# Kernel optimization log

Hardware: AMD Instinct MI355X
Metric: run time of the kernel (lower is better)

## Reference

```python
import jax, jax.numpy as jnp
import numpy as np

N, H, W, KB, CTRL, MEM, L, NMOD = 256, 14, 14, 512, 512, 512, 8, 9
TEMP = 1.0
EPS = 1e-12


def _l2norm(x):
    # torch F.normalize(p=2, dim=-1, eps=1e-12)
    return x / jnp.maximum(jnp.linalg.norm(x, axis=-1, keepdims=True), EPS)


def _spatial_softmax(att):  # [N,H,W,1]
    n = att.shape[0]
    return jax.nn.softmax(att.reshape(n, -1), axis=1).reshape(att.shape)


def _extract_softmax_avg(kb, att_raw):  # -> [N,KB]
    return (kb * _spatial_softmax(att_raw)).sum((1, 2))


def _move_bw(ptr):
    # conv1d with kernel [0,0,1], pad 1 => shift left (pop); guard keeps mass at slot 0
    new = jnp.pad(ptr[:, 1:], ((0, 0), (0, 1)))
    return new.at[:, 0].add(ptr[:, 0])


def _move_fw(ptr):
    # conv1d with kernel [1,0,0], pad 1 => shift right (push); guard keeps mass at slot L-1
    new = jnp.pad(ptr[:, :-1], ((0, 0), (1, 0)))
    return new.at[:, -1].add(ptr[:, -1])


def _read(stk, ptr):  # [N,H,W,L],[N,L] -> [N,H,W,1]
    return (stk * ptr[:, None, None, :]).sum(-1, keepdims=True)


def _write(stk, ptr, att):
    p = ptr[:, None, None, :]
    return att * p + stk * (1.0 - p)


def _sharpen(ptr):
    return jax.nn.softmax(ptr / TEMP, axis=1)


def setup_inputs() -> dict:
    key = jax.random.key(0)
    ks = jax.random.split(key, 16)

    def lin(k, fan_in, shape):
        return (jax.random.normal(k, shape, jnp.float32) / np.sqrt(fan_in)).astype(jnp.float32)

    u_ptr = jax.random.uniform(ks[0], (N, L), jnp.float32)
    u_mod = jax.random.uniform(ks[1], (N, NMOD), jnp.float32)
    C2 = 2 * KB + CTRL
    return {
        "control_state": jax.random.normal(ks[2], (N, CTRL), jnp.float32),
        "kb_batch": jax.random.normal(ks[3], (N, H, W, KB), jnp.float32),
        "module_prob": u_mod / u_mod.sum(1, keepdims=True),
        "mem_prev": jax.random.normal(ks[4], (N, MEM), jnp.float32),
        "att_stack_prev": jax.random.uniform(ks[5], (N, H, W, L), jnp.float32),
        "stack_ptr_prev": u_ptr / u_ptr.sum(1, keepdims=True),
        "find_ci_w": lin(ks[6], CTRL, (CTRL, KB)), "find_ci_b": jnp.zeros((KB,), jnp.float32),
        "find_conv_w": lin(ks[7], KB, (KB, 1)), "find_conv_b": jnp.zeros((1,), jnp.float32),
        "transform_ci_w": lin(ks[8], CTRL, (CTRL, KB)), "transform_ci_b": jnp.zeros((KB,), jnp.float32),
        "transform_conv_w": lin(ks[9], KB, (KB, 1)), "transform_conv_b": jnp.zeros((1,), jnp.float32),
        "scene_conv_w": lin(ks[10], KB, (KB, 1)), "scene_conv_b": jnp.zeros((1,), jnp.float32),
        "describeone_ci_w": lin(ks[11], CTRL, (CTRL, KB)), "describeone_ci_b": jnp.zeros((KB,), jnp.float32),
        "describeone_mem_w": lin(ks[12], C2, (C2, MEM)), "describeone_mem_b": jnp.zeros((MEM,), jnp.float32),
        "describetwo_ci_w": lin(ks[13], CTRL, (CTRL, KB)), "describetwo_ci_b": jnp.zeros((KB,), jnp.float32),
        "describetwo_mem_w": lin(ks[14], C2, (C2, MEM)), "describetwo_mem_b": jnp.zeros((MEM,), jnp.float32),
    }


def reference(control_state, kb_batch, module_prob, mem_prev, att_stack_prev, stack_ptr_prev,
              find_ci_w, find_ci_b, find_conv_w, find_conv_b,
              transform_ci_w, transform_ci_b, transform_conv_w, transform_conv_b,
              scene_conv_w, scene_conv_b,
              describeone_ci_w, describeone_ci_b, describeone_mem_w, describeone_mem_b,
              describetwo_ci_w, describetwo_ci_b, describetwo_mem_w, describetwo_mem_b):
    mem_zero = jnp.zeros_like(mem_prev)

    def NoOp(stk, ptr):
        return stk, ptr, mem_prev

    def Find(stk, ptr):
        c = control_state @ find_ci_w + find_ci_b  # [N,KB]
        elt = _l2norm(kb_batch * c[:, None, None, :])
        att = elt @ find_conv_w + find_conv_b  # 1x1 conv on channels-last -> [N,H,W,1]
        ptr = _move_fw(ptr)
        return _write(stk, ptr, att), ptr, mem_zero

    def Transform(stk, ptr):
        att_in = _read(stk, ptr)
        c = control_state @ transform_ci_w + transform_ci_b
        kb_att = _extract_softmax_avg(kb_batch, att_in)
        elt = _l2norm(kb_batch * c[:, None, None, :] * kb_att[:, None, None, :])
        att = elt @ transform_conv_w + transform_conv_b
        return _write(stk, ptr, att), ptr, mem_zero

    def And(stk, ptr):
        att2 = _read(stk, ptr)
        ptr = _move_bw(ptr)
        att1 = _read(stk, ptr)
        return _write(stk, ptr, jnp.minimum(att1, att2)), ptr, mem_zero

    def Or(stk, ptr):
        att2 = _read(stk, ptr)
        ptr = _move_bw(ptr)
        att1 = _read(stk, ptr)
        return _write(stk, ptr, jnp.maximum(att1, att2)), ptr, mem_zero

    def Filter(stk, ptr):
        stk, ptr, _ = Find(stk, ptr)
        stk, ptr, _ = And(stk, ptr)
        return stk, ptr, mem_zero

    def Scene(stk, ptr):
        att = _l2norm(kb_batch) @ scene_conv_w + scene_conv_b
        ptr = _move_fw(ptr)
        return _write(stk, ptr, att), ptr, mem_zero

    def DescribeOne(stk, ptr):
        att_in = _read(stk, ptr)
        c = control_state @ describeone_ci_w + describeone_ci_b
        kb_att = _extract_softmax_avg(kb_batch, att_in)
        elt = _l2norm(c * kb_att)
        mem = jnp.concatenate([control_state, elt, kb_att], axis=1) @ describeone_mem_w + describeone_mem_b
        return stk, ptr, mem

    def DescribeTwo(stk, ptr):
        att2 = _read(stk, ptr)
        ptr = _move_bw(ptr)
        att1 = _read(stk, ptr)
        c = control_state @ describetwo_ci_w + describetwo_ci_b
        kb_att1 = _extract_softmax_avg(kb_batch, att1)
        kb_att2 = _extract_softmax_avg(kb_batch, att2)
        elt = _l2norm(c * kb_att1 * kb_att2)
        mem = jnp.concatenate([control_state, elt, kb_att1], axis=1) @ describetwo_mem_w + describetwo_mem_b
        stk = _write(stk, ptr, jnp.minimum(att1, att2))
        return stk, ptr, mem

    funcs = [NoOp, Find, Transform, Filter, And, Or, Scene, DescribeOne, DescribeTwo]
    res = [f(att_stack_prev, stack_ptr_prev) for f in funcs]  # fixed small set of modules
    stks = jnp.stack([r[0] for r in res], axis=-1)  # [N,H,W,L,M]
    ptrs = jnp.stack([r[1] for r in res], axis=-1)  # [N,L,M]
    mems = jnp.stack([r[2] for r in res], axis=-1)  # [N,MEM,M]
    att_stack_avg = (module_prob[:, None, None, None, :] * stks).sum(-1)
    stack_ptr_avg = _sharpen((module_prob[:, None, :] * ptrs).sum(-1))
    mem_avg = (module_prob[:, None, :] * mems).sum(-1)
    return att_stack_avg, stack_ptr_avg, mem_avg
```

## Files before the change

kernel.cpp:

```cpp
#include <hip/hip_runtime.h>
#include <math.h>

constexpr int   NB   = 256;
constexpr int   HW   = 196;
constexpr int   KBC  = 512;
constexpr int   LSZ  = 8;
constexpr float EPSF = 1e-12f;

constexpr size_t S_ATT    = (size_t)NB * HW;
constexpr size_t OFF_ATT1 = 0;
constexpr size_t OFF_ATT2 = OFF_ATT1 + S_ATT;
constexpr size_t OFF_W1   = OFF_ATT2 + S_ATT;
constexpr size_t OFF_W2   = OFF_W1   + S_ATT;
constexpr size_t OFF_AF   = OFF_W2   + S_ATT;
constexpr size_t OFF_AT   = OFF_AF   + S_ATT;
constexpr size_t OFF_AS   = OFF_AT   + S_ATT;
constexpr size_t OFF_C1   = OFF_AS   + S_ATT;
constexpr size_t OFF_A1   = OFF_C1 + (size_t)NB*2048;
constexpr size_t OFF_A2   = OFF_A1 + (size_t)NB*1536;
constexpr size_t OFF_G    = OFF_A2 + (size_t)NB*1536;
constexpr size_t OFF_SCR  = OFF_G  + (size_t)NB*512;
constexpr size_t OFF_PF   = OFF_SCR + 1048576 + 131072;
constexpr size_t OFF_PB   = OFF_PF   + (size_t)NB*LSZ;
constexpr size_t OFF_PFB  = OFF_PB   + (size_t)NB*LSZ;
constexpr size_t OFF_SF2  = OFF_PFB  + (size_t)NB*LSZ;
constexpr size_t OFF_SFFB = OFF_SF2  + NB;
constexpr size_t WS_FLOATS= OFF_SFFB + NB;

static __device__ __forceinline__ float4 ld4(const float* p) {
    return *reinterpret_cast<const float4*>(p);
}

__global__ __launch_bounds__(256) void k_att(
    const float* __restrict__ stk, const float* __restrict__ ptrp,
    float* __restrict__ att1g, float* __restrict__ att2g,
    float* __restrict__ w1g, float* __restrict__ w2g,
    float* __restrict__ fws, float* __restrict__ bws, float* __restrict__ fbws,
    float* __restrict__ sf2ws, float* __restrict__ sffbws)
{
    const int n = blockIdx.x;
    const int t = threadIdx.x;
    float pp[8], f[8], b[8], fb[8];
#pragma unroll
    for (int l = 0; l < 8; ++l) pp[l] = ptrp[n*8 + l];
    f[0] = 0.f;
#pragma unroll
    for (int l = 1; l < 8; ++l) f[l] = pp[l-1];
    f[7] += pp[7];
#pragma unroll
    for (int l = 0; l < 7; ++l) b[l] = pp[l+1];
    b[7] = 0.f;
    b[0] += pp[0];
#pragma unroll
    for (int l = 0; l < 7; ++l) fb[l] = f[l+1];
    fb[7] = 0.f;
    fb[0] += f[0];

    if (t == 0) {
        float sf2 = 0.f, sffb = 0.f;
#pragma unroll
        for (int l = 0; l < 8; ++l) {
            fws[n*8+l] = f[l]; bws[n*8+l] = b[l]; fbws[n*8+l] = fb[l];
            sf2  += f[l]*f[l];
            sffb += f[l]*fb[l];
        }
        sf2ws[n] = sf2; sffbws[n] = sffb;
    }

    float a1 = 0.f, a2 = 0.f;
    if (t < HW) {
        const float* sp = stk + ((size_t)n*HW + t) * 8;
        float4 v0 = ld4(sp), v1 = ld4(sp + 4);
        float s[8] = {v0.x, v0.y, v0.z, v0.w, v1.x, v1.y, v1.z, v1.w};
#pragma unroll
        for (int l = 0; l < 8; ++l) {
            a2 = fmaf(s[l], pp[l], a2);
            a1 = fmaf(s[l],  b[l], a1);
        }
        att1g[n*HW + t] = a1;
        att2g[n*HW + t] = a2;
    }

    __shared__ float red[256];
    red[t] = (t < HW) ? a1 : -3.0e38f;
    __syncthreads();
    for (int off = 128; off > 0; off >>= 1) { if (t < off) red[t] = fmaxf(red[t], red[t+off]); __syncthreads(); }
    const float m1 = red[0];
    __syncthreads();
    float e1 = (t < HW) ? __expf(a1 - m1) : 0.f;
    red[t] = e1;
    __syncthreads();
    for (int off = 128; off > 0; off >>= 1) { if (t < off) red[t] += red[t+off]; __syncthreads(); }
    const float s1 = red[0];
    __syncthreads();
    if (t < HW) w1g[n*HW + t] = e1 / s1;

    red[t] = (t < HW) ? a2 : -3.0e38f;
    __syncthreads();
    for (int off = 128; off > 0; off >>= 1) { if (t < off) red[t] = fmaxf(red[t], red[t+off]); __syncthreads(); }
    const float m2 = red[0];
    __syncthreads();
    float e2 = (t < HW) ? __expf(a2 - m2) : 0.f;
    red[t] = e2;
    __syncthreads();
    for (int off = 128; off > 0; off >>= 1) { if (t < off) red[t] += red[t+off]; __syncthreads(); }
    const float s2 = red[0];
    __syncthreads();
    if (t < HW) w2g[n*HW + t] = e2 / s2;
}

template<int KCHUNK, bool SELKS, int ASTR, int NTOT>
__global__ __launch_bounds__(256) void gemm_sk(
    const float* __restrict__ A0, const float* __restrict__ A1p,
    const float* __restrict__ B0, const float* __restrict__ B1,
    const float* __restrict__ B2, const float* __restrict__ B3,
    float* __restrict__ P)
{
    const int t  = threadIdx.x;
    const int tx = t & 15, ty = t >> 4;
    const int bn = blockIdx.x * 64;
    const int bm = blockIdx.y * 64;
    const int ks = blockIdx.z;

    const float* A; const float* B; int kbase; int bcol;
    if constexpr (SELKS) {
        const int mat = ks >> 2;
        A = mat ? A1p : A0;
        B = mat ? B1 : B0;
        kbase = ks * KCHUNK - mat * (4 * KCHUNK);
        bcol = bn;
    } else {
        const int mat = bn >> 9;
        A = A0;
        B = (mat == 0) ? B0 : (mat == 1) ? B1 : (mat == 2) ? B2 : B3;
        kbase = ks * KCHUNK;
        bcol = bn & 511;
    }
    constexpr int NT = KCHUNK / 16;

    __shared__ float As[16][68];
    __shared__ float Bs[16][68];
    float acc[4][4] = {};

    const int ar = t >> 2, ac4 = (t & 3) * 4;
    const int br = t >> 4, bc4 = (t & 15) * 4;
    const float* Aptr = A + (size_t)(bm + ar) * ASTR + kbase + ac4;
    const float* Bptr = B + (size_t)(kbase + br) * 512 + bcol + bc4;

    float4 aR = ld4(Aptr), bR = ld4(Bptr);
    for (int tile = 0; tile < NT; ++tile) {
        As[ac4+0][ar] = aR.x; As[ac4+1][ar] = aR.y; As[ac4+2][ar] = aR.z; As[ac4+3][ar] = aR.w;
        *reinterpret_cast<float4*>(&Bs[br][bc4]) = bR;
        __syncthreads();
        if (tile + 1 < NT) {
            aR = ld4(Aptr + (tile+1)*16);
            bR = ld4(Bptr + (size_t)(tile+1)*16*512);
        }
#pragma unroll
        for (int k = 0; k < 16; ++k) {
            float4 ra = *reinterpret_cast<const float4*>(&As[k][ty*4]);
            float4 rb = *reinterpret_cast<const float4*>(&Bs[k][tx*4]);
            const float av[4] = {ra.x, ra.y, ra.z, ra.w};
            const float bv[4] = {rb.x, rb.y, rb.z, rb.w};
#pragma unroll
            for (int i = 0; i < 4; ++i)
#pragma unroll
                for (int j = 0; j < 4; ++j)
                    acc[i][j] = fmaf(av[i], bv[j], acc[i][j]);
        }
        __syncthreads();
    }
#pragma unroll
    for (int i = 0; i < 4; ++i) {
        float4 v = make_float4(acc[i][0], acc[i][1], acc[i][2], acc[i][3]);
        *reinterpret_cast<float4*>(&P[((size_t)ks*NB + bm + ty*4 + i) * NTOT + bn + tx*4]) = v;
    }
}

__global__ __launch_bounds__(256) void k_red1(
    const float* __restrict__ P,
    const float* __restrict__ b0, const float* __restrict__ b1,
    const float* __restrict__ b2, const float* __restrict__ b3,
    float* __restrict__ C1)
{
    const size_t q = ((size_t)blockIdx.x * 256 + threadIdx.x) * 4;
    const int c = (int)(q & 2047);
    float4 s0 = ld4(P + q);
    float4 s1 = ld4(P + 524288 + q);
    float4 s2 = ld4(P + 2*524288 + q);
    float4 s3 = ld4(P + 3*524288 + q);
    const int mat = c >> 9, cl = c & 511;
    const float* bb = (mat == 0) ? b0 : (mat == 1) ? b1 : (mat == 2) ? b2 : b3;
    float4 o;
    o.x = s0.x + s1.x + s2.x + s3.x + bb[cl+0];
    o.y = s0.y + s1.y + s2.y + s3.y + bb[cl+1];
    o.z = s0.z + s1.z + s2.z + s3.z + bb[cl+2];
    o.w = s0.w + s1.w + s2.w + s3.w + bb[cl+3];
    *reinterpret_cast<float4*>(&C1[q]) = o;
}

__global__ __launch_bounds__(256) void k_kbA(
    const float* __restrict__ kb, const float* __restrict__ C1,
    const float* __restrict__ w_find, const float* __restrict__ b_find,
    const float* __restrict__ w_scene, const float* __restrict__ b_scene,
    const float* __restrict__ w1g, const float* __restrict__ w2g,
    float* __restrict__ aF, float* __restrict__ aS, float* __restrict__ kpart)
{
    const int blk = blockIdx.x;
    const int n = blk >> 2, sp = blk & 3;
    const int t = threadIdx.x, wv = t >> 6, lane = t & 63;
    const int k0 = lane * 8;
    const int p0 = sp * 49;

    __shared__ float w1s[49], w2s[49];
    __shared__ float kred[4][1024];
    if (t < 49) { w1s[t] = w1g[n*HW + p0 + t]; w2s[t] = w2g[n*HW + p0 + t]; }
    __syncthreads();

    float cf[8], wf[8], wsc[8];
    {
        float4 a0 = ld4(C1 + (size_t)n*2048 + k0), a1 = ld4(C1 + (size_t)n*2048 + k0 + 4);
        cf[0]=a0.x; cf[1]=a0.y; cf[2]=a0.z; cf[3]=a0.w; cf[4]=a1.x; cf[5]=a1.y; cf[6]=a1.z; cf[7]=a1.w;
        float4 b0 = ld4(w_find + k0), b1 = ld4(w_find + k0 + 4);
        wf[0]=b0.x; wf[1]=b0.y; wf[2]=b0.z; wf[3]=b0.w; wf[4]=b1.x; wf[5]=b1.y; wf[6]=b1.z; wf[7]=b1.w;
        float4 c0 = ld4(w_scene + k0), c1 = ld4(w_scene + k0 + 4);
        wsc[0]=c0.x; wsc[1]=c0.y; wsc[2]=c0.z; wsc[3]=c0.w; wsc[4]=c1.x; wsc[5]=c1.y; wsc[6]=c1.z; wsc[7]=c1.w;
    }
    const float bf = b_find[0], bs = b_scene[0];

    float k1a[8] = {0,0,0,0,0,0,0,0};
    float k2a[8] = {0,0,0,0,0,0,0,0};

    for (int pl = wv; pl < 49; pl += 4) {
        const float* src = kb + (((size_t)n*HW + p0 + pl) * KBC + k0);
        float4 v0 = ld4(src), v1 = ld4(src + 4);
        float kv[8] = {v0.x, v0.y, v0.z, v0.w, v1.x, v1.y, v1.z, v1.w};
        float sA = 0.f, sB = 0.f, sE = 0.f, sF = 0.f;
#pragma unroll
        for (int j = 0; j < 8; ++j) {
            const float t1 = kv[j] * cf[j];
            sA = fmaf(t1, t1, sA);
            sB = fmaf(t1, wf[j], sB);
            sE = fmaf(kv[j], kv[j], sE);
            sF = fmaf(kv[j], wsc[j], sF);
        }
        const float w1p = w1s[pl], w2p = w2s[pl];
#pragma unroll
        for (int j = 0; j < 8; ++j) {
            k1a[j] = fmaf(w1p, kv[j], k1a[j]);
            k2a[j] = fmaf(w2p, kv[j], k2a[j]);
        }
#pragma unroll
        for (int m = 1; m < 64; m <<= 1) {
            sA += __shfl_xor(sA, m);
            sB += __shfl_xor(sB, m);
            sE += __shfl_xor(sE, m);
            sF += __shfl_xor(sF, m);
        }
        if (lane == 0) {
            const size_t p = (size_t)n*HW + p0 + pl;
            aF[p] = sB / fmaxf(sqrtf(sA), EPSF) + bf;
            aS[p] = sF / fmaxf(sqrtf(sE), EPSF) + bs;
        }
    }
#pragma unroll
    for (int j = 0; j < 8; ++j) { kred[wv][k0 + j] = k1a[j]; kred[wv][512 + k0 + j] = k2a[j]; }
    __syncthreads();
    for (int idx = t; idx < 1024; idx += 256) {
        const float s = kred[0][idx] + kred[1][idx] + kred[2][idx] + kred[3][idx];
        kpart[((size_t)sp*NB + n) * 1024 + idx] = s;
    }
}

__global__ __launch_bounds__(256) void k_elt(
    const float* __restrict__ kpart, const float* __restrict__ C1,
    const float* __restrict__ control, const float* __restrict__ prob,
    float* __restrict__ g, float* __restrict__ A1, float* __restrict__ A2)
{
    const int n = blockIdx.x;
    const int t = threadIdx.x;
    __shared__ float k1s[512], k2s[512];
    for (int idx = t; idx < 512; idx += 256) {
        float s1 = 0.f, s2 = 0.f;
#pragma unroll
        for (int sp = 0; sp < 4; ++sp) {
            const float* base = kpart + ((size_t)sp*NB + n) * 1024;
            s1 += base[idx];
            s2 += base[512 + idx];
        }
        k1s[idx] = s1; k2s[idx] = s2;
    }
    __syncthreads();

    float v1[2], v2[2];
    float sum1 = 0.f, sum2 = 0.f;
#pragma unroll
    for (int i = 0; i < 2; ++i) {
        const int k = t + i*256;
        const float ct  = C1[(size_t)n*2048 + 512  + k];
        const float cd1 = C1[(size_t)n*2048 + 1024 + k];
        const float cd2 = C1[(size_t)n*2048 + 1536 + k];
        g[(size_t)n*512 + k] = ct * k2s[k];
        v1[i] = cd1 * k2s[k];
        v2[i] = cd2 * k1s[k] * k2s[k];
        sum1 = fmaf(v1[i], v1[i], sum1);
        sum2 = fmaf(v2[i], v2[i], sum2);
    }
    __shared__ float r1[256], r2[256];
    r1[t] = sum1; r2[t] = sum2;
    __syncthreads();
    for (int off = 128; off > 0; off >>= 1) {
        if (t < off) { r1[t] += r1[t+off]; r2[t] += r2[t+off]; }
        __syncthreads();
    }
    const float n1 = fmaxf(sqrtf(r1[0]), EPSF);
    const float n2 = fmaxf(sqrtf(r2[0]), EPSF);
    const float p7 = prob[n*9 + 7], p8 = prob[n*9 + 8];
#pragma unroll
    for (int i = 0; i < 2; ++i) {
        const int k = t + i*256;
        const float c = control[(size_t)n*512 + k];
        A1[(size_t)n*1536 + k]        = p7 * c;
        A1[(size_t)n*1536 + 512 + k]  = p7 * v1[i] / n1;
        A1[(size_t)n*1536 + 1024 + k] = p7 * k2s[k];
        A2[(size_t)n*1536 + k]        = p8 * c;
        A2[(size_t)n*1536 + 512 + k]  = p8 * v2[i] / n2;
        A2[(size_t)n*1536 + 1024 + k] = p8 * k1s[k];
    }
}

__global__ __launch_bounds__(256) void k_kbB(
    const float* __restrict__ kb, const float* __restrict__ g,
    const float* __restrict__ w_tr, const float* __restrict__ b_tr,
    float* __restrict__ aT)
{
    const int blk = blockIdx.x;
    const int n = blk >> 2, sp = blk & 3;
    const int t = threadIdx.x, wv = t >> 6, lane = t & 63;
    const int k0 = lane * 8;
    const int p0 = sp * 49;
    float gv[8], wt[8];
    {
        float4 a0 = ld4(g + (size_t)n*512 + k0), a1 = ld4(g + (size_t)n*512 + k0 + 4);
        gv[0]=a0.x; gv[1]=a0.y; gv[2]=a0.z; gv[3]=a0.w; gv[4]=a1.x; gv[5]=a1.y; gv[6]=a1.z; gv[7]=a1.w;
        float4 b0 = ld4(w_tr + k0), b1 = ld4(w_tr + k0 + 4);
        wt[0]=b0.x; wt[1]=b0.y; wt[2]=b0.z; wt[3]=b0.w; wt[4]=b1.x; wt[5]=b1.y; wt[6]=b1.z; wt[7]=b1.w;
    }
    const float bt = b_tr[0];
    for (int pl = wv; pl < 49; pl += 4) {
        const float* src = kb + (((size_t)n*HW + p0 + pl) * KBC + k0);
        float4 v0 = ld4(src), v1 = ld4(src + 4);
        float kv[8] = {v0.x, v0.y, v0.z, v0.w, v1.x, v1.y, v1.z, v1.w};
        float sC = 0.f, sD = 0.f;
#pragma unroll
        for (int j = 0; j < 8; ++j) {
            const float u = kv[j] * gv[j];
            sC = fmaf(u, u, sC);
            sD = fmaf(u, wt[j], sD);
        }
#pragma unroll
        for (int m = 1; m < 64; m <<= 1) { sC += __shfl_xor(sC, m); sD += __shfl_xor(sD, m); }
        if (lane == 0) aT[(size_t)n*HW + p0 + pl] = sD / fmaxf(sqrtf(sC), EPSF) + bt;
    }
}

__global__ __launch_bounds__(256) void k_memout(
    const float* __restrict__ P2, const float* __restrict__ memprev,
    const float* __restrict__ prob,
    const float* __restrict__ b1, const float* __restrict__ b2,
    float* __restrict__ out_mem)
{
    const size_t q = ((size_t)blockIdx.x * 256 + threadIdx.x) * 4;
    const int n = (int)(q >> 9), j = (int)(q & 511);
    const float p0 = prob[n*9 + 0], p7 = prob[n*9 + 7], p8 = prob[n*9 + 8];
    float4 s = ld4(P2 + q);
#pragma unroll
    for (int sp = 1; sp < 8; ++sp) {
        float4 v = ld4(P2 + (size_t)sp*131072 + q);
        s.x += v.x; s.y += v.y; s.z += v.z; s.w += v.w;
    }
    float4 mp = ld4(memprev + q);
    float4 w1 = ld4(b1 + j), w2 = ld4(b2 + j);
    float4 o;
    o.x = p0*mp.x + s.x + p7*w1.x + p8*w2.x;
    o.y = p0*mp.y + s.y + p7*w1.y + p8*w2.y;
    o.z = p0*mp.z + s.z + p7*w1.z + p8*w2.z;
    o.w = p0*mp.w + s.w + p7*w1.w + p8*w2.w;
    *reinterpret_cast<float4*>(&out_mem[q]) = o;
}

__global__ __launch_bounds__(256) void k_assemble(
    const float* __restrict__ stk, const float* __restrict__ ptrp,
    const float* __restrict__ prob,
    const float* __restrict__ att1g, const float* __restrict__ att2g,
    const float* __restrict__ aFg, const float* __restrict__ aTg, const float* __restrict__ aSg,
    const float* __restrict__ fws, const float* __restrict__ bws, const float* __restrict__ fbws,
    const float* __restrict__ sf2ws, const float* __restrict__ sffbws,
    float* __restrict__ out_att, float* __restrict__ out_ptr)
{
    const int n = blockIdx.x;
    const int t = threadIdx.x;
    __shared__ float pp[8], f[8], b[8], fb[8], pr[9], sc2[2];
    if (t < 8) { pp[t] = ptrp[n*8+t]; f[t] = fws[n*8+t]; b[t] = bws[n*8+t]; fb[t] = fbws[n*8+t]; }
    if (t < 9) pr[t] = prob[n*9+t];
    if (t == 0) { sc2[0] = sf2ws[n]; sc2[1] = sffbws[n]; }
    __syncthreads();

    if (t < HW) {
        const size_t p = (size_t)n*HW + t;
        const float* spt = stk + p*8;
        float4 v0 = ld4(spt), v1 = ld4(spt+4);
        float s[8] = {v0.x, v0.y, v0.z, v0.w, v1.x, v1.y, v1.z, v1.w};
        const float a1 = att1g[p], a2 = att2g[p];
        const float vaF = aFg[p], vaT = aTg[p], vaS = aSg[p];
        const float mn = fminf(a1, a2), mx = fmaxf(a1, a2);
        float rf = 0.f, rf2 = 0.f, rfb = 0.f, rffb = 0.f;
#pragma unroll
        for (int l = 0; l < 8; ++l) {
            rf   = fmaf(s[l], f[l],        rf);
            rf2  = fmaf(s[l], f[l]*f[l],   rf2);
            rfb  = fmaf(s[l], fb[l],       rfb);
            rffb = fmaf(s[l], f[l]*fb[l],  rffb);
        }
        const float att2p = vaF*sc2[0] + rf  - rf2;
        const float att1p = vaF*sc2[1] + rfb - rffb;
        const float mnF = fminf(att1p, att2p);
        const float c48 = pr[4] + pr[8];
        float o[8];
#pragma unroll
        for (int l = 0; l < 8; ++l) {
            const float sl = s[l];
            const float stkF = vaF*f[l] + sl*(1.f - f[l]);
            float r = (pr[0] + pr[7]) * sl;
            r = fmaf(pr[1], stkF, r);
            r = fmaf(pr[2], vaT*pp[l] + sl*(1.f - pp[l]), r);
            r = fmaf(pr[3], mnF*fb[l] + stkF*(1.f - fb[l]), r);
            r = fmaf(c48,   mn*b[l] + sl*(1.f - b[l]), r);
            r = fmaf(pr[5], mx*b[l] + sl*(1.f - b[l]), r);
            r = fmaf(pr[6], vaS*f[l] + sl*(1.f - f[l]), r);
            o[l] = r;
        }
        *reinterpret_cast<float4*>(out_att + p*8)     = make_float4(o[0], o[1], o[2], o[3]);
        *reinterpret_cast<float4*>(out_att + p*8 + 4) = make_float4(o[4], o[5], o[6], o[7]);
    }

    if (t == 0) {
        const float cpp = pr[0] + pr[2] + pr[7];
        const float cf  = pr[1] + pr[6];
        const float cb  = pr[4] + pr[5] + pr[8];
        float pa[8];
        float m = -3.0e38f;
#pragma unroll
        for (int l = 0; l < 8; ++l) {
            pa[l] = cpp*pp[l] + cf*f[l] + cb*b[l] + pr[3]*fb[l];
            m = fmaxf(m, pa[l]);
        }
        float ssum = 0.f;
#pragma unroll
        for (int l = 0; l < 8; ++l) { pa[l] = __expf(pa[l] - m); ssum += pa[l]; }
#pragma unroll
        for (int l = 0; l < 8; ++l) out_ptr[n*8 + l] = pa[l] / ssum;
    }
}

extern "C" void kernel_launch(void* const* d_in, const int* in_sizes, int n_in,
                              void* d_out, int out_size, void* d_ws, size_t ws_size,
                              hipStream_t stream)
{
    (void)in_sizes; (void)n_in; (void)out_size;
    const float* control = (const float*)d_in[0];
    const float* kb      = (const float*)d_in[1];
    const float* prob    = (const float*)d_in[2];
    const float* memprev = (const float*)d_in[3];
    const float* stk     = (const float*)d_in[4];
    const float* ptrp    = (const float*)d_in[5];
    const float* find_w  = (const float*)d_in[6];
    const float* find_b  = (const float*)d_in[7];
    const float* findc_w = (const float*)d_in[8];
    const float* findc_b = (const float*)d_in[9];
    const float* tr_w    = (const float*)d_in[10];
    const float* tr_b    = (const float*)d_in[11];
    const float* trc_w   = (const float*)d_in[12];
    const float* trc_b   = (const float*)d_in[13];
    const float* sc_w    = (const float*)d_in[14];
    const float* sc_b    = (const float*)d_in[15];
    const float* d1_w    = (const float*)d_in[16];
    const float* d1_b    = (const float*)d_in[17];
    const float* d1m_w   = (const float*)d_in[18];
    const float* d1m_b   = (const float*)d_in[19];
    const float* d2_w    = (const float*)d_in[20];
    const float* d2_b    = (const float*)d_in[21];
    const float* d2m_w   = (const float*)d_in[22];
    const float* d2m_b   = (const float*)d_in[23];

    if (ws_size < WS_FLOATS * sizeof(float)) return;

    float* ws    = (float*)d_ws;
    float* att1g = ws + OFF_ATT1;
    float* att2g = ws + OFF_ATT2;
    float* w1g   = ws + OFF_W1;
    float* w2g   = ws + OFF_W2;
    float* aF    = ws + OFF_AF;
    float* aT    = ws + OFF_AT;
    float* aS    = ws + OFF_AS;
    float* C1    = ws + OFF_C1;
    float* A1    = ws + OFF_A1;
    float* A2    = ws + OFF_A2;
    float* g     = ws + OFF_G;
    float* scr   = ws + OFF_SCR;
    float* GP1   = ws + OFF_A1;
    float* fws   = ws + OFF_PF;
    float* bws   = ws + OFF_PB;
    float* fbws  = ws + OFF_PFB;
    float* sf2   = ws + OFF_SF2;
    float* sffb  = ws + OFF_SFFB;

    float* out_att = (float*)d_out;
    float* out_ptr = out_att + (size_t)NB*HW*LSZ;
    float* out_mem = out_ptr + (size_t)NB*LSZ;

    k_att<<<NB, 256, 0, stream>>>(stk, ptrp, att1g, att2g, w1g, w2g,
                                  fws, bws, fbws, sf2, sffb);
    gemm_sk<128, false, 512, 2048><<<dim3(32, 4, 4), 256, 0, stream>>>(
        control, nullptr, find_w, tr_w, d1_w, d2_w, GP1);
    k_red1<<<512, 256, 0, stream>>>(GP1, find_b, tr_b, d1_b, d2_b, C1);
    k_kbA<<<NB*4, 256, 0, stream>>>(kb, C1, findc_w, findc_b, sc_w, sc_b,
                                    w1g, w2g, aF, aS, scr);
    k_elt<<<NB, 256, 0, stream>>>(scr, C1, control, prob, g, A1, A2);
    k_kbB<<<NB*4, 256, 0, stream>>>(kb, g, trc_w, trc_b, aT);
    gemm_sk<384, true, 1536, 512><<<dim3(8, 4, 8), 256, 0, stream>>>(
        A1, A2, d1m_w, d2m_w, nullptr, nullptr, scr);
    k_memout<<<128, 256, 0, stream>>>(scr, memprev, prob, d1m_b, d2m_b, out_mem);
    k_assemble<<<NB, 256, 0, stream>>>(stk, ptrp, prob, att1g, att2g, aF, aT, aS,
                                       fws, bws, fbws, sf2, sffb, out_att, out_ptr);
}
```

Before: 92.55 us.

## Merge independent kernels into shared launches and fold split-K reductions into consumers

```diff
diff --git a/kernel.cpp b/kernel.cpp
--- a/kernel.cpp
+++ b/kernel.cpp
@@ -15,12 +15,13 @@
 constexpr size_t OFF_AF   = OFF_W2   + S_ATT;
 constexpr size_t OFF_AT   = OFF_AF   + S_ATT;
 constexpr size_t OFF_AS   = OFF_AT   + S_ATT;
-constexpr size_t OFF_C1   = OFF_AS   + S_ATT;
-constexpr size_t OFF_A1   = OFF_C1 + (size_t)NB*2048;
-constexpr size_t OFF_A2   = OFF_A1 + (size_t)NB*1536;
-constexpr size_t OFF_G    = OFF_A2 + (size_t)NB*1536;
-constexpr size_t OFF_SCR  = OFF_G  + (size_t)NB*512;
-constexpr size_t OFF_PF   = OFF_SCR + 1048576 + 131072;
+constexpr size_t OFF_GP1  = OFF_AS   + S_ATT;
+constexpr size_t OFF_KP   = OFF_GP1  + (size_t)4*NB*2048;
+constexpr size_t OFF_A1   = OFF_KP   + (size_t)4*NB*1024;
+constexpr size_t OFF_A2   = OFF_A1   + (size_t)NB*1536;
+constexpr size_t OFF_G    = OFF_A2   + (size_t)NB*1536;
+constexpr size_t OFF_P2   = OFF_G    + (size_t)NB*512;
+constexpr size_t OFF_PF   = OFF_P2   + (size_t)16*NB*512;
 constexpr size_t OFF_PB   = OFF_PF   + (size_t)NB*LSZ;
 constexpr size_t OFF_PFB  = OFF_PB   + (size_t)NB*LSZ;
 constexpr size_t OFF_SF2  = OFF_PFB  + (size_t)NB*LSZ;
@@ -31,128 +32,115 @@
     return *reinterpret_cast<const float4*>(p);
 }
 
-__global__ __launch_bounds__(256) void k_att(
+__global__ __launch_bounds__(256) void k_front(
     const float* __restrict__ stk, const float* __restrict__ ptrp,
     float* __restrict__ att1g, float* __restrict__ att2g,
     float* __restrict__ w1g, float* __restrict__ w2g,
     float* __restrict__ fws, float* __restrict__ bws, float* __restrict__ fbws,
-    float* __restrict__ sf2ws, float* __restrict__ sffbws)
-{
-    const int n = blockIdx.x;
-    const int t = threadIdx.x;
-    float pp[8], f[8], b[8], fb[8];
-#pragma unroll
-    for (int l = 0; l < 8; ++l) pp[l] = ptrp[n*8 + l];
-    f[0] = 0.f;
-#pragma unroll
-    for (int l = 1; l < 8; ++l) f[l] = pp[l-1];
-    f[7] += pp[7];
-#pragma unroll
-    for (int l = 0; l < 7; ++l) b[l] = pp[l+1];
-    b[7] = 0.f;
-    b[0] += pp[0];
-#pragma unroll
-    for (int l = 0; l < 7; ++l) fb[l] = f[l+1];
-    fb[7] = 0.f;
-    fb[0] += f[0];
-
-    if (t == 0) {
-        float sf2 = 0.f, sffb = 0.f;
-#pragma unroll
-        for (int l = 0; l < 8; ++l) {
-            fws[n*8+l] = f[l]; bws[n*8+l] = b[l]; fbws[n*8+l] = fb[l];
-            sf2  += f[l]*f[l];
-            sffb += f[l]*fb[l];
-        }
-        sf2ws[n] = sf2; sffbws[n] = sffb;
-    }
-
-    float a1 = 0.f, a2 = 0.f;
-    if (t < HW) {
-        const float* sp = stk + ((size_t)n*HW + t) * 8;
-        float4 v0 = ld4(sp), v1 = ld4(sp + 4);
-        float s[8] = {v0.x, v0.y, v0.z, v0.w, v1.x, v1.y, v1.z, v1.w};
-#pragma unroll
-        for (int l = 0; l < 8; ++l) {
-            a2 = fmaf(s[l], pp[l], a2);
-            a1 = fmaf(s[l],  b[l], a1);
-        }
-        att1g[n*HW + t] = a1;
-        att2g[n*HW + t] = a2;
-    }
-
-    __shared__ float red[256];
-    red[t] = (t < HW) ? a1 : -3.0e38f;
-    __syncthreads();
-    for (int off = 128; off > 0; off >>= 1) { if (t < off) red[t] = fmaxf(red[t], red[t+off]); __syncthreads(); }
-    const float m1 = red[0];
-    __syncthreads();
-    float e1 = (t < HW) ? __expf(a1 - m1) : 0.f;
-    red[t] = e1;
-    __syncthreads();
-    for (int off = 128; off > 0; off >>= 1) { if (t < off) red[t] += red[t+off]; __syncthreads(); }
-    const float s1 = red[0];
-    __syncthreads();
-    if (t < HW) w1g[n*HW + t] = e1 / s1;
-
-    red[t] = (t < HW) ? a2 : -3.0e38f;
-    __syncthreads();
-    for (int off = 128; off > 0; off >>= 1) { if (t < off) red[t] = fmaxf(red[t], red[t+off]); __syncthreads(); }
-    const float m2 = red[0];
-    __syncthreads();
-    float e2 = (t < HW) ? __expf(a2 - m2) : 0.f;
-    red[t] = e2;
-    __syncthreads();
-    for (int off = 128; off > 0; off >>= 1) { if (t < off) red[t] += red[t+off]; __syncthreads(); }
-    const float s2 = red[0];
-    __syncthreads();
-    if (t < HW) w2g[n*HW + t] = e2 / s2;
-}
-
-template<int KCHUNK, bool SELKS, int ASTR, int NTOT>
-__global__ __launch_bounds__(256) void gemm_sk(
-    const float* __restrict__ A0, const float* __restrict__ A1p,
+    float* __restrict__ sf2ws, float* __restrict__ sffbws,
+    const float* __restrict__ control,
     const float* __restrict__ B0, const float* __restrict__ B1,
     const float* __restrict__ B2, const float* __restrict__ B3,
-    float* __restrict__ P)
+    float* __restrict__ GP1)
 {
-    const int t  = threadIdx.x;
-    const int tx = t & 15, ty = t >> 4;
-    const int bn = blockIdx.x * 64;
-    const int bm = blockIdx.y * 64;
-    const int ks = blockIdx.z;
-
-    const float* A; const float* B; int kbase; int bcol;
-    if constexpr (SELKS) {
-        const int mat = ks >> 2;
-        A = mat ? A1p : A0;
-        B = mat ? B1 : B0;
-        kbase = ks * KCHUNK - mat * (4 * KCHUNK);
-        bcol = bn;
-    } else {
-        const int mat = bn >> 9;
-        A = A0;
-        B = (mat == 0) ? B0 : (mat == 1) ? B1 : (mat == 2) ? B2 : B3;
-        kbase = ks * KCHUNK;
-        bcol = bn & 511;
-    }
-    constexpr int NT = KCHUNK / 16;
-
+    __shared__ float red[256];
     __shared__ float As[16][68];
     __shared__ float Bs[16][68];
+    const int t = threadIdx.x;
+
+    if (blockIdx.x < 256) {
+        const int n = blockIdx.x;
+        float pp[8], f[8], b[8], fb[8];
+#pragma unroll
+        for (int l = 0; l < 8; ++l) pp[l] = ptrp[n*8 + l];
+        f[0] = 0.f;
+#pragma unroll
+        for (int l = 1; l < 8; ++l) f[l] = pp[l-1];
+        f[7] += pp[7];
+#pragma unroll
+        for (int l = 0; l < 7; ++l) b[l] = pp[l+1];
+        b[7] = 0.f;
+        b[0] += pp[0];
+#pragma unroll
+        for (int l = 0; l < 7; ++l) fb[l] = f[l+1];
+        fb[7] = 0.f;
+        fb[0] += f[0];
+
+        if (t == 0) {
+            float sf2 = 0.f, sffb = 0.f;
+#pragma unroll
+            for (int l = 0; l < 8; ++l) {
+                fws[n*8+l] = f[l]; bws[n*8+l] = b[l]; fbws[n*8+l] = fb[l];
+                sf2  += f[l]*f[l];
+                sffb += f[l]*fb[l];
+            }
+            sf2ws[n] = sf2; sffbws[n] = sffb;
+        }
+
+        float a1 = 0.f, a2 = 0.f;
+        if (t < HW) {
+            const float* sp = stk + ((size_t)n*HW + t) * 8;
+            float4 v0 = ld4(sp), v1 = ld4(sp + 4);
+            float s[8] = {v0.x, v0.y, v0.z, v0.w, v1.x, v1.y, v1.z, v1.w};
+#pragma unroll
+            for (int l = 0; l < 8; ++l) {
+                a2 = fmaf(s[l], pp[l], a2);
+                a1 = fmaf(s[l],  b[l], a1);
+            }
+            att1g[n*HW + t] = a1;
+            att2g[n*HW + t] = a2;
+        }
+
+        red[t] = (t < HW) ? a1 : -3.0e38f;
+        __syncthreads();
+        for (int off = 128; off > 0; off >>= 1) { if (t < off) red[t] = fmaxf(red[t], red[t+off]); __syncthreads(); }
+        const float m1 = red[0];
+        __syncthreads();
+        float e1 = (t < HW) ? __expf(a1 - m1) : 0.f;
+        red[t] = e1;
+        __syncthreads();
+        for (int off = 128; off > 0; off >>= 1) { if (t < off) red[t] += red[t+off]; __syncthreads(); }
+        const float s1 = red[0];
+        __syncthreads();
+        if (t < HW) w1g[n*HW + t] = e1 / s1;
+
+        red[t] = (t < HW) ? a2 : -3.0e38f;
+        __syncthreads();
+        for (int off = 128; off > 0; off >>= 1) { if (t < off) red[t] = fmaxf(red[t], red[t+off]); __syncthreads(); }
+        const float m2 = red[0];
+        __syncthreads();
+        float e2 = (t < HW) ? __expf(a2 - m2) : 0.f;
+        red[t] = e2;
+        __syncthreads();
+        for (int off = 128; off > 0; off >>= 1) { if (t < off) red[t] += red[t+off]; __syncthreads(); }
+        const float s2 = red[0];
+        __syncthreads();
+        if (t < HW) w2g[n*HW + t] = e2 / s2;
+        return;
+    }
+
+    const int idx = blockIdx.x - 256;
+    const int bn = (idx & 31) * 64;
+    const int bm = ((idx >> 5) & 3) * 64;
+    const int ks = idx >> 7;
+    const int mat = bn >> 9;
+    const float* B = (mat == 0) ? B0 : (mat == 1) ? B1 : (mat == 2) ? B2 : B3;
+    const int kbase = ks * 128;
+    const int bcol = bn & 511;
+
+    const int tx = t & 15, ty = t >> 4;
     float acc[4][4] = {};
-
     const int ar = t >> 2, ac4 = (t & 3) * 4;
     const int br = t >> 4, bc4 = (t & 15) * 4;
-    const float* Aptr = A + (size_t)(bm + ar) * ASTR + kbase + ac4;
+    const float* Aptr = control + (size_t)(bm + ar) * 512 + kbase + ac4;
     const float* Bptr = B + (size_t)(kbase + br) * 512 + bcol + bc4;
 
     float4 aR = ld4(Aptr), bR = ld4(Bptr);
-    for (int tile = 0; tile < NT; ++tile) {
+    for (int tile = 0; tile < 8; ++tile) {
         As[ac4+0][ar] = aR.x; As[ac4+1][ar] = aR.y; As[ac4+2][ar] = aR.z; As[ac4+3][ar] = aR.w;
         *reinterpret_cast<float4*>(&Bs[br][bc4]) = bR;
         __syncthreads();
-        if (tile + 1 < NT) {
+        if (tile + 1 < 8) {
             aR = ld4(Aptr + (tile+1)*16);
             bR = ld4(Bptr + (size_t)(tile+1)*16*512);
         }
@@ -173,34 +161,13 @@
 #pragma unroll
     for (int i = 0; i < 4; ++i) {
         float4 v = make_float4(acc[i][0], acc[i][1], acc[i][2], acc[i][3]);
-        *reinterpret_cast<float4*>(&P[((size_t)ks*NB + bm + ty*4 + i) * NTOT + bn + tx*4]) = v;
-    }
-}
-
-__global__ __launch_bounds__(256) void k_red1(
-    const float* __restrict__ P,
-    const float* __restrict__ b0, const float* __restrict__ b1,
-    const float* __restrict__ b2, const float* __restrict__ b3,
-    float* __restrict__ C1)
-{
-    const size_t q = ((size_t)blockIdx.x * 256 + threadIdx.x) * 4;
-    const int c = (int)(q & 2047);
-    float4 s0 = ld4(P + q);
-    float4 s1 = ld4(P + 524288 + q);
-    float4 s2 = ld4(P + 2*524288 + q);
-    float4 s3 = ld4(P + 3*524288 + q);
-    const int mat = c >> 9, cl = c & 511;
-    const float* bb = (mat == 0) ? b0 : (mat == 1) ? b1 : (mat == 2) ? b2 : b3;
-    float4 o;
-    o.x = s0.x + s1.x + s2.x + s3.x + bb[cl+0];
-    o.y = s0.y + s1.y + s2.y + s3.y + bb[cl+1];
-    o.z = s0.z + s1.z + s2.z + s3.z + bb[cl+2];
-    o.w = s0.w + s1.w + s2.w + s3.w + bb[cl+3];
-    *reinterpret_cast<float4*>(&C1[q]) = o;
+        *reinterpret_cast<float4*>(&GP1[((size_t)ks*NB + bm + ty*4 + i) * 2048 + bn + tx*4]) = v;
+    }
 }
 
 __global__ __launch_bounds__(256) void k_kbA(
-    const float* __restrict__ kb, const float* __restrict__ C1,
+    const float* __restrict__ kb, const float* __restrict__ GP1,
+    const float* __restrict__ find_ci_b,
     const float* __restrict__ w_find, const float* __restrict__ b_find,
     const float* __restrict__ w_scene, const float* __restrict__ b_scene,
     const float* __restrict__ w1g, const float* __restrict__ w2g,
@@ -219,21 +186,34 @@
 
     float cf[8], wf[8], wsc[8];
     {
-        float4 a0 = ld4(C1 + (size_t)n*2048 + k0), a1 = ld4(C1 + (size_t)n*2048 + k0 + 4);
-        cf[0]=a0.x; cf[1]=a0.y; cf[2]=a0.z; cf[3]=a0.w; cf[4]=a1.x; cf[5]=a1.y; cf[6]=a1.z; cf[7]=a1.w;
-        float4 b0 = ld4(w_find + k0), b1 = ld4(w_find + k0 + 4);
-        wf[0]=b0.x; wf[1]=b0.y; wf[2]=b0.z; wf[3]=b0.w; wf[4]=b1.x; wf[5]=b1.y; wf[6]=b1.z; wf[7]=b1.w;
-        float4 c0 = ld4(w_scene + k0), c1 = ld4(w_scene + k0 + 4);
-        wsc[0]=c0.x; wsc[1]=c0.y; wsc[2]=c0.z; wsc[3]=c0.w; wsc[4]=c1.x; wsc[5]=c1.y; wsc[6]=c1.z; wsc[7]=c1.w;
+        const float* gp = GP1 + (size_t)n*2048 + k0;
+        float4 a0 = ld4(gp),            a1 = ld4(gp + 4);
+        float4 b0 = ld4(gp + 524288),   b1 = ld4(gp + 524288 + 4);
+        float4 c0 = ld4(gp + 1048576),  c1 = ld4(gp + 1048576 + 4);
+        float4 d0 = ld4(gp + 1572864),  d1 = ld4(gp + 1572864 + 4);
+        float4 e0 = ld4(find_ci_b + k0), e1 = ld4(find_ci_b + k0 + 4);
+        cf[0]=a0.x+b0.x+c0.x+d0.x+e0.x; cf[1]=a0.y+b0.y+c0.y+d0.y+e0.y;
+        cf[2]=a0.z+b0.z+c0.z+d0.z+e0.z; cf[3]=a0.w+b0.w+c0.w+d0.w+e0.w;
+        cf[4]=a1.x+b1.x+c1.x+d1.x+e1.x; cf[5]=a1.y+b1.y+c1.y+d1.y+e1.y;
+        cf[6]=a1.z+b1.z+c1.z+d1.z+e1.z; cf[7]=a1.w+b1.w+c1.w+d1.w+e1.w;
+        float4 f0 = ld4(w_find + k0), f1 = ld4(w_find + k0 + 4);
+        wf[0]=f0.x; wf[1]=f0.y; wf[2]=f0.z; wf[3]=f0.w; wf[4]=f1.x; wf[5]=f1.y; wf[6]=f1.z; wf[7]=f1.w;
+        float4 g0 = ld4(w_scene + k0), g1 = ld4(w_scene + k0 + 4);
+        wsc[0]=g0.x; wsc[1]=g0.y; wsc[2]=g0.z; wsc[3]=g0.w; wsc[4]=g1.x; wsc[5]=g1.y; wsc[6]=g1.z; wsc[7]=g1.w;
     }
     const float bf = b_find[0], bs = b_scene[0];
 
     float k1a[8] = {0,0,0,0,0,0,0,0};
     float k2a[8] = {0,0,0,0,0,0,0,0};
 
+    const float* src0 = kb + (((size_t)n*HW + p0 + wv) * KBC + k0);
+    float4 v0 = ld4(src0), v1 = ld4(src0 + 4);
     for (int pl = wv; pl < 49; pl += 4) {
-        const float* src = kb + (((size_t)n*HW + p0 + pl) * KBC + k0);
-        float4 v0 = ld4(src), v1 = ld4(src + 4);
+        float4 n0, n1;
+        if (pl + 4 < 49) {
+            const float* ns = kb + (((size_t)n*HW + p0 + pl + 4) * KBC + k0);
+            n0 = ld4(ns); n1 = ld4(ns + 4);
+        }
         float kv[8] = {v0.x, v0.y, v0.z, v0.w, v1.x, v1.y, v1.z, v1.w};
         float sA = 0.f, sB = 0.f, sE = 0.f, sF = 0.f;
 #pragma unroll
@@ -262,6 +242,7 @@
             aF[p] = sB / fmaxf(sqrtf(sA), EPSF) + bf;
             aS[p] = sF / fmaxf(sqrtf(sE), EPSF) + bs;
         }
+        v0 = n0; v1 = n1;
     }
 #pragma unroll
     for (int j = 0; j < 8; ++j) { kred[wv][k0 + j] = k1a[j]; kred[wv][512 + k0 + j] = k2a[j]; }
@@ -273,7 +254,9 @@
 }
 
 __global__ __launch_bounds__(256) void k_elt(
-    const float* __restrict__ kpart, const float* __restrict__ C1,
+    const float* __restrict__ kpart, const float* __restrict__ GP1,
+    const float* __restrict__ tr_ci_b, const float* __restrict__ d1_ci_b,
+    const float* __restrict__ d2_ci_b,
     const float* __restrict__ control, const float* __restrict__ prob,
     float* __restrict__ g, float* __restrict__ A1, float* __restrict__ A2)
 {
@@ -297,9 +280,10 @@
 #pragma unroll
     for (int i = 0; i < 2; ++i) {
         const int k = t + i*256;
-        const float ct  = C1[(size_t)n*2048 + 512  + k];
-        const float cd1 = C1[(size_t)n*2048 + 1024 + k];
-        const float cd2 = C1[(size_t)n*2048 + 1536 + k];
+        const float* gp = GP1 + (size_t)n*2048 + k;
+        const float ct  = gp[512]  + gp[524288+512]  + gp[1048576+512]  + gp[1572864+512]  + tr_ci_b[k];
+        const float cd1 = gp[1024] + gp[524288+1024] + gp[1048576+1024] + gp[1572864+1024] + d1_ci_b[k];
+        const float cd2 = gp[1536] + gp[524288+1536] + gp[1048576+1536] + gp[1572864+1536] + d2_ci_b[k];
         g[(size_t)n*512 + k] = ct * k2s[k];
         v1[i] = cd1 * k2s[k];
         v2[i] = cd2 * k1s[k] * k2s[k];
@@ -329,77 +313,137 @@
     }
 }
 
-__global__ __launch_bounds__(256) void k_kbB(
+__global__ __launch_bounds__(256) void k_mid(
     const float* __restrict__ kb, const float* __restrict__ g,
     const float* __restrict__ w_tr, const float* __restrict__ b_tr,
-    float* __restrict__ aT)
+    float* __restrict__ aT,
+    const float* __restrict__ A1, const float* __restrict__ A2,
+    const float* __restrict__ W1, const float* __restrict__ W2,
+    float* __restrict__ P2)
 {
-    const int blk = blockIdx.x;
-    const int n = blk >> 2, sp = blk & 3;
-    const int t = threadIdx.x, wv = t >> 6, lane = t & 63;
-    const int k0 = lane * 8;
-    const int p0 = sp * 49;
-    float gv[8], wt[8];
-    {
-        float4 a0 = ld4(g + (size_t)n*512 + k0), a1 = ld4(g + (size_t)n*512 + k0 + 4);
-        gv[0]=a0.x; gv[1]=a0.y; gv[2]=a0.z; gv[3]=a0.w; gv[4]=a1.x; gv[5]=a1.y; gv[6]=a1.z; gv[7]=a1.w;
-        float4 b0 = ld4(w_tr + k0), b1 = ld4(w_tr + k0 + 4);
-        wt[0]=b0.x; wt[1]=b0.y; wt[2]=b0.z; wt[3]=b0.w; wt[4]=b1.x; wt[5]=b1.y; wt[6]=b1.z; wt[7]=b1.w;
-    }
-    const float bt = b_tr[0];
-    for (int pl = wv; pl < 49; pl += 4) {
-        const float* src = kb + (((size_t)n*HW + p0 + pl) * KBC + k0);
-        float4 v0 = ld4(src), v1 = ld4(src + 4);
-        float kv[8] = {v0.x, v0.y, v0.z, v0.w, v1.x, v1.y, v1.z, v1.w};
-        float sC = 0.f, sD = 0.f;
-#pragma unroll
-        for (int j = 0; j < 8; ++j) {
-            const float u = kv[j] * gv[j];
-            sC = fmaf(u, u, sC);
-            sD = fmaf(u, wt[j], sD);
-        }
-#pragma unroll
-        for (int m = 1; m < 64; m <<= 1) { sC += __shfl_xor(sC, m); sD += __shfl_xor(sD, m); }
-        if (lane == 0) aT[(size_t)n*HW + p0 + pl] = sD / fmaxf(sqrtf(sC), EPSF) + bt;
-    }
-}
-
-__global__ __launch_bounds__(256) void k_memout(
+    __shared__ float As[16][68];
+    __shared__ float Bs[16][68];
+    const int t = threadIdx.x;
+
+    if (blockIdx.x < 1024) {
+        const int blk = blockIdx.x;
+        const int n = blk >> 2, sp = blk & 3;
+        const int wv = t >> 6, lane = t & 63;
+        const int k0 = lane * 8;
+        const int p0 = sp * 49;
+        float gv[8], wt[8];
+        {
+            float4 a0 = ld4(g + (size_t)n*512 + k0), a1 = ld4(g + (size_t)n*512 + k0 + 4);
+            gv[0]=a0.x; gv[1]=a0.y; gv[2]=a0.z; gv[3]=a0.w; gv[4]=a1.x; gv[5]=a1.y; gv[6]=a1.z; gv[7]=a1.w;
+            float4 b0 = ld4(w_tr + k0), b1 = ld4(w_tr + k0 + 4);
+            wt[0]=b0.x; wt[1]=b0.y; wt[2]=b0.z; wt[3]=b0.w; wt[4]=b1.x; wt[5]=b1.y; wt[6]=b1.z; wt[7]=b1.w;
+        }
+        const float bt = b_tr[0];
+        const float* src0 = kb + (((size_t)n*HW + p0 + wv) * KBC + k0);
+        float4 v0 = ld4(src0), v1 = ld4(src0 + 4);
+        for (int pl = wv; pl < 49; pl += 4) {
+            float4 n0, n1;
+            if (pl + 4 < 49) {
+                const float* ns = kb + (((size_t)n*HW + p0 + pl + 4) * KBC + k0);
+                n0 = ld4(ns); n1 = ld4(ns + 4);
+            }
+            float kv[8] = {v0.x, v0.y, v0.z, v0.w, v1.x, v1.y, v1.z, v1.w};
+            float sC = 0.f, sD = 0.f;
+#pragma unroll
+            for (int j = 0; j < 8; ++j) {
+                const float u = kv[j] * gv[j];
+                sC = fmaf(u, u, sC);
+                sD = fmaf(u, wt[j], sD);
+            }
+#pragma unroll
+            for (int m = 1; m < 64; m <<= 1) { sC += __shfl_xor(sC, m); sD += __shfl_xor(sD, m); }
+            if (lane == 0) aT[(size_t)n*HW + p0 + pl] = sD / fmaxf(sqrtf(sC), EPSF) + bt;
+            v0 = n0; v1 = n1;
+        }
+        return;
+    }
+
+    const int idx = blockIdx.x - 1024;
+    const int bn = (idx & 7) * 64;
+    const int bm = ((idx >> 3) & 3) * 64;
+    const int ks = idx >> 5;
+    const int mat = ks >> 3;
+    const float* A = mat ? A2 : A1;
+    const float* B = mat ? W2 : W1;
+    const int kbase = ks * 192 - mat * 1536;
+
+    const int tx = t & 15, ty = t >> 4;
+    float acc[4][4] = {};
+    const int ar = t >> 2, ac4 = (t & 3) * 4;
+    const int br = t >> 4, bc4 = (t & 15) * 4;
+    const float* Aptr = A + (size_t)(bm + ar) * 1536 + kbase + ac4;
+    const float* Bptr = B + (size_t)(kbase + br) * 512 + bn + bc4;
+
+    float4 aR = ld4(Aptr), bR = ld4(Bptr);
+    for (int tile = 0; tile < 12; ++tile) {
+        As[ac4+0][ar] = aR.x; As[ac4+1][ar] = aR.y; As[ac4+2][ar] = aR.z; As[ac4+3][ar] = aR.w;
+        *reinterpret_cast<float4*>(&Bs[br][bc4]) = bR;
+        __syncthreads();
+        if (tile + 1 < 12) {
+            aR = ld4(Aptr + (tile+1)*16);
+            bR = ld4(Bptr + (size_t)(tile+1)*16*512);
+        }
+#pragma unroll
+        for (int k = 0; k < 16; ++k) {
+            float4 ra = *reinterpret_cast<const float4*>(&As[k][ty*4]);
+            float4 rb = *reinterpret_cast<const float4*>(&Bs[k][tx*4]);
+            const float av[4] = {ra.x, ra.y, ra.z, ra.w};
+            const float bv[4] = {rb.x, rb.y, rb.z, rb.w};
+#pragma unroll
+            for (int i = 0; i < 4; ++i)
+#pragma unroll
+                for (int j = 0; j < 4; ++j)
+                    acc[i][j] = fmaf(av[i], bv[j], acc[i][j]);
+        }
+        __syncthreads();
+    }
+#pragma unroll
+    for (int i = 0; i < 4; ++i) {
+        float4 v = make_float4(acc[i][0], acc[i][1], acc[i][2], acc[i][3]);
+        *reinterpret_cast<float4*>(&P2[((size_t)ks*NB + bm + ty*4 + i) * 512 + bn + tx*4]) = v;
+    }
+}
+
+__global__ __launch_bounds__(256) void k_back(
     const float* __restrict__ P2, const float* __restrict__ memprev,
     const float* __restrict__ prob,
-    const float* __restrict__ b1, const float* __restrict__ b2,
-    float* __restrict__ out_mem)
-{
-    const size_t q = ((size_t)blockIdx.x * 256 + threadIdx.x) * 4;
-    const int n = (int)(q >> 9), j = (int)(q & 511);
-    const float p0 = prob[n*9 + 0], p7 = prob[n*9 + 7], p8 = prob[n*9 + 8];
-    float4 s = ld4(P2 + q);
-#pragma unroll
-    for (int sp = 1; sp < 8; ++sp) {
-        float4 v = ld4(P2 + (size_t)sp*131072 + q);
-        s.x += v.x; s.y += v.y; s.z += v.z; s.w += v.w;
-    }
-    float4 mp = ld4(memprev + q);
-    float4 w1 = ld4(b1 + j), w2 = ld4(b2 + j);
-    float4 o;
-    o.x = p0*mp.x + s.x + p7*w1.x + p8*w2.x;
-    o.y = p0*mp.y + s.y + p7*w1.y + p8*w2.y;
-    o.z = p0*mp.z + s.z + p7*w1.z + p8*w2.z;
-    o.w = p0*mp.w + s.w + p7*w1.w + p8*w2.w;
-    *reinterpret_cast<float4*>(&out_mem[q]) = o;
-}
-
-__global__ __launch_bounds__(256) void k_assemble(
+    const float* __restrict__ mb1, const float* __restrict__ mb2,
+    float* __restrict__ out_mem,
     const float* __restrict__ stk, const float* __restrict__ ptrp,
-    const float* __restrict__ prob,
     const float* __restrict__ att1g, const float* __restrict__ att2g,
     const float* __restrict__ aFg, const float* __restrict__ aTg, const float* __restrict__ aSg,
     const float* __restrict__ fws, const float* __restrict__ bws, const float* __restrict__ fbws,
     const float* __restrict__ sf2ws, const float* __restrict__ sffbws,
     float* __restrict__ out_att, float* __restrict__ out_ptr)
 {
-    const int n = blockIdx.x;
     const int t = threadIdx.x;
+    if (blockIdx.x < 128) {
+        const size_t q = ((size_t)blockIdx.x * 256 + t) * 4;
+        const int n = (int)(q >> 9), j = (int)(q & 511);
+        const float p0 = prob[n*9 + 0], p7 = prob[n*9 + 7], p8 = prob[n*9 + 8];
+        float4 s = ld4(P2 + q);
+#pragma unroll
+        for (int sp = 1; sp < 16; ++sp) {
+            float4 v = ld4(P2 + (size_t)sp*131072 + q);
+            s.x += v.x; s.y += v.y; s.z += v.z; s.w += v.w;
+        }
+        float4 mp = ld4(memprev + q);
+        float4 w1 = ld4(mb1 + j), w2 = ld4(mb2 + j);
+        float4 o;
+        o.x = p0*mp.x + s.x + p7*w1.x + p8*w2.x;
+        o.y = p0*mp.y + s.y + p7*w1.y + p8*w2.y;
+        o.z = p0*mp.z + s.z + p7*w1.z + p8*w2.z;
+        o.w = p0*mp.w + s.w + p7*w1.w + p8*w2.w;
+        *reinterpret_cast<float4*>(&out_mem[q]) = o;
+        return;
+    }
+
+    const int n = blockIdx.x - 128;
     __shared__ float pp[8], f[8], b[8], fb[8], pr[9], sc2[2];
     if (t < 8) { pp[t] = ptrp[n*8+t]; f[t] = fws[n*8+t]; b[t] = bws[n*8+t]; fb[t] = fbws[n*8+t]; }
     if (t < 9) pr[t] = prob[n*9+t];
@@ -503,12 +547,12 @@
     float* aF    = ws + OFF_AF;
     float* aT    = ws + OFF_AT;
     float* aS    = ws + OFF_AS;
-    float* C1    = ws + OFF_C1;
+    float* GP1   = ws + OFF_GP1;
+    float* kpart = ws + OFF_KP;
     float* A1    = ws + OFF_A1;
     float* A2    = ws + OFF_A2;
     float* g     = ws + OFF_G;
-    float* scr   = ws + OFF_SCR;
-    float* GP1   = ws + OFF_A1;
+    float* P2    = ws + OFF_P2;
     float* fws   = ws + OFF_PF;
     float* bws   = ws + OFF_PB;
     float* fbws  = ws + OFF_PFB;
@@ -519,18 +563,16 @@
     float* out_ptr = out_att + (size_t)NB*HW*LSZ;
     float* out_mem = out_ptr + (size_t)NB*LSZ;
 
-    k_att<<<NB, 256, 0, stream>>>(stk, ptrp, att1g, att2g, w1g, w2g,
-                                  fws, bws, fbws, sf2, sffb);
-    gemm_sk<128, false, 512, 2048><<<dim3(32, 4, 4), 256, 0, stream>>>(
-        control, nullptr, find_w, tr_w, d1_w, d2_w, GP1);
-    k_red1<<<512, 256, 0, stream>>>(GP1, find_b, tr_b, d1_b, d2_b, C1);
-    k_kbA<<<NB*4, 256, 0, stream>>>(kb, C1, findc_w, findc_b, sc_w, sc_b,
-                                    w1g, w2g, aF, aS, scr);
-    k_elt<<<NB, 256, 0, stream>>>(scr, C1, control, prob, g, A1, A2);
-    k_kbB<<<NB*4, 256, 0, stream>>>(kb, g, trc_w, trc_b, aT);
-    gemm_sk<384, true, 1536, 512><<<dim3(8, 4, 8), 256, 0, stream>>>(
-        A1, A2, d1m_w, d2m_w, nullptr, nullptr, scr);
-    k_memout<<<128, 256, 0, stream>>>(scr, memprev, prob, d1m_b, d2m_b, out_mem);
-    k_assemble<<<NB, 256, 0, stream>>>(stk, ptrp, prob, att1g, att2g, aF, aT, aS,
-                                       fws, bws, fbws, sf2, sffb, out_att, out_ptr);
-}
+    k_front<<<256 + 512, 256, 0, stream>>>(
+        stk, ptrp, att1g, att2g, w1g, w2g, fws, bws, fbws, sf2, sffb,
+        control, find_w, tr_w, d1_w, d2_w, GP1);
+    k_kbA<<<NB*4, 256, 0, stream>>>(kb, GP1, find_b, findc_w, findc_b, sc_w, sc_b,
+                                    w1g, w2g, aF, aS, kpart);
+    k_elt<<<NB, 256, 0, stream>>>(kpart, GP1, tr_b, d1_b, d2_b,
+                                  control, prob, g, A1, A2);
+    k_mid<<<1024 + 512, 256, 0, stream>>>(kb, g, trc_w, trc_b, aT,
+                                          A1, A2, d1m_w, d2m_w, P2);
+    k_back<<<128 + 256, 256, 0, stream>>>(P2, memprev, prob, d1m_b, d2m_b, out_mem,
+                                          stk, ptrp, att1g, att2g, aF, aT, aS,
+                                          fws, bws, fbws, sf2, sffb, out_att, out_ptr);
+}
```

Measured after the change: 78.50 us, median of 2. 1.18x faster.
